# Kernel tuning notes

Measured on AMD Instinct MI355X. Metric: run time of the kernel, lower is better.

The kernel has to match this reference:

```python
import jax, jax.numpy as jnp
import numpy as np

DIM = 1024
NUM_HEADS = 16
HEAD_DIM = DIM // NUM_HEADS
B, L = 2, 2048


def setup_inputs() -> dict:
    key = jax.random.key(0)
    k_x, k_qkv, k_pw, k_pb = jax.random.split(key, 4)
    x = jax.random.normal(k_x, (B, L, DIM), dtype=jnp.float32)
    # nn.Linear(dim, 3*dim, bias=False): weight [3*dim, dim]; y = x @ W.T
    w_qkv = jax.random.normal(k_qkv, (3 * DIM, DIM), dtype=jnp.float32) * (DIM ** -0.5)
    # nn.Linear(dim, dim) with bias
    w_proj = jax.random.normal(k_pw, (DIM, DIM), dtype=jnp.float32) * (DIM ** -0.5)
    b_proj = jax.random.normal(k_pb, (DIM,), dtype=jnp.float32) * 0.01
    return {"x": x, "w_qkv": w_qkv, "w_proj": w_proj, "b_proj": b_proj}


def reference(x, w_qkv, w_proj, b_proj):
    Bx, Lx, C = x.shape
    qkv = x @ w_qkv.T  # [B, L, 3C]
    qkv = qkv.reshape(Bx, Lx, 3, NUM_HEADS, HEAD_DIM)
    q = jnp.transpose(qkv[:, :, 0], (0, 2, 1, 3))  # [B, H, L, D]
    k = jnp.transpose(qkv[:, :, 1], (0, 2, 1, 3))
    v = jnp.transpose(qkv[:, :, 2], (0, 2, 1, 3))
    attn = jnp.einsum('bhqd,bhkd->bhqk', q, k) * (HEAD_DIM ** -0.5)
    attn = jax.nn.softmax(attn, axis=-1)
    out = jnp.einsum('bhqk,bhkd->bhqd', attn, v)  # [B, H, L, D]
    out = jnp.transpose(out, (0, 2, 1, 3)).reshape(Bx, Lx, C)
    return out @ w_proj.T + b_proj
```

## Files before the change

### kernel.cpp

```cpp
#include <hip/hip_runtime.h>

#define DIM 1024
#define NH 16
#define HD 64
#define BB 2
#define LL 2048
#define BL (BB*LL)
#define NQKV (3*DIM)

typedef __bf16 bf16;
typedef __bf16 bf16x4 __attribute__((ext_vector_type(4)));
typedef __bf16 bf16x8 __attribute__((ext_vector_type(8)));
typedef float  f32x4  __attribute__((ext_vector_type(4)));

#define QSCALE 0.1803368801111204f

typedef __attribute__((address_space(3))) unsigned int lds_u32;
typedef __attribute__((address_space(1))) unsigned int glb_u32;

__device__ __forceinline__ void gld_lds16(const bf16* g, bf16* l) {
    __builtin_amdgcn_global_load_lds((const glb_u32*)g, (lds_u32*)l, 16, 0, 0);
}

#define C0 (BL*DIM/4)
#define C1 (NQKV*DIM/4)
#define C2 (DIM*DIM/4)
__global__ __launch_bounds__(256) void cvt_all(const float* __restrict__ x,
        const float* __restrict__ wq, const float* __restrict__ wp,
        bf16* __restrict__ xb, bf16* __restrict__ wqb, bf16* __restrict__ wpb) {
    int i = blockIdx.x * 256 + threadIdx.x;
    const float* in; bf16* out; int j;
    if (i < C0)            { in = x;  out = xb;  j = i; }
    else if (i < C0 + C1)  { in = wq; out = wqb; j = i - C0; }
    else                   { in = wp; out = wpb; j = i - C0 - C1; }
    float4 f = ((const float4*)in)[j];
    bf16x4 o = { (bf16)f.x, (bf16)f.y, (bf16)f.z, (bf16)f.w };
    ((bf16x4*)out)[j] = o;
}

__global__ __launch_bounds__(256, 3) void gemm_qkv(
        const bf16* __restrict__ A, const bf16* __restrict__ W,
        bf16* __restrict__ Qb, bf16* __restrict__ Kb, bf16* __restrict__ VTb) {
    __shared__ bf16 As[128][64];
    __shared__ bf16 Bs[128][64];
    const int tid = threadIdx.x;
    const int w = tid >> 6, lane = tid & 63, quad = lane >> 4, l16 = lane & 15;
    const int n0 = blockIdx.x * 128, m0 = blockIdx.y * 128;
    const int wm = (w & 1) * 64, wn = (w >> 1) * 64;
    f32x4 acc[4][4] = {};
    for (int k0 = 0; k0 < DIM; k0 += 64) {
        #pragma unroll
        for (int i = 0; i < 4; ++i) {
            int cb = w * 256 + i * 64;
            int gc = cb + lane;
            int r = gc >> 3;
            int cs = (gc & 7) ^ (r & 7);
            gld_lds16(A + (size_t)(m0 + r) * DIM + k0 + cs*8, &As[0][0] + cb * 8);
            gld_lds16(W + (size_t)(n0 + r) * DIM + k0 + cs*8, &Bs[0][0] + cb * 8);
        }
        __syncthreads();
        #pragma unroll
        for (int kc = 0; kc < 2; ++kc) {
            bf16x8 af[4], bfr[4];
            #pragma unroll
            for (int t = 0; t < 4; ++t) {
                int rw = wn + t*16 + l16;
                int cw = (kc*4 + quad) ^ (rw & 7);
                af[t] = *(const bf16x8*)(&Bs[0][0] + rw*64 + cw*8);
                int rx = wm + t*16 + l16;
                int cx = (kc*4 + quad) ^ (rx & 7);
                bfr[t] = *(const bf16x8*)(&As[0][0] + rx*64 + cx*8);
            }
            #pragma unroll
            for (int tm = 0; tm < 4; ++tm)
                #pragma unroll
                for (int tn = 0; tn < 4; ++tn)
                    acc[tm][tn] = __builtin_amdgcn_mfma_f32_16x16x32_bf16(
                                      af[tm], bfr[tn], acc[tm][tn], 0, 0, 0);
        }
        __syncthreads();
    }
    const int which = n0 >> 10;
    #pragma unroll
    for (int tm = 0; tm < 4; ++tm) {
        int nb = n0 + wn + tm*16 + quad*4;
        int rem = nb & 1023, h = rem >> 6, db = rem & 63;
        #pragma unroll
        for (int tn = 0; tn < 4; ++tn) {
            int m = m0 + wm + tn*16 + l16;
            int b = m >> 11, l = m & 2047, bh = (b << 4) | h;
            if (which == 0) {
                bf16x4 q4 = { (bf16)(acc[tm][tn][0] * QSCALE),
                              (bf16)(acc[tm][tn][1] * QSCALE),
                              (bf16)(acc[tm][tn][2] * QSCALE),
                              (bf16)(acc[tm][tn][3] * QSCALE) };
                *(bf16x4*)(Qb + ((size_t)bh << 17) + ((size_t)l << 6) + db) = q4;
            } else if (which == 1) {
                bf16x4 k4 = { (bf16)acc[tm][tn][0], (bf16)acc[tm][tn][1],
                              (bf16)acc[tm][tn][2], (bf16)acc[tm][tn][3] };
                *(bf16x4*)(Kb + ((size_t)bh << 17) + ((size_t)l << 6) + db) = k4;
            } else {
                #pragma unroll
                for (int r = 0; r < 4; ++r)
                    VTb[((size_t)bh << 17) + ((size_t)(db + r) << 11) + l] =
                        (bf16)acc[tm][tn][r];
            }
        }
    }
}

__global__ __launch_bounds__(256, 3) void gemm_proj(
        const bf16* __restrict__ A, const bf16* __restrict__ W,
        const float* __restrict__ bias, float* __restrict__ out) {
    __shared__ bf16 As[128][64];
    __shared__ bf16 Bs[64][64];
    const int tid = threadIdx.x;
    const int w = tid >> 6, lane = tid & 63, quad = lane >> 4, l16 = lane & 15;
    const int n0 = blockIdx.x * 64, m0 = blockIdx.y * 128;
    const int wm = (w & 1) * 64, wn = (w >> 1) * 32;
    f32x4 acc[2][4] = {};
    for (int k0 = 0; k0 < DIM; k0 += 64) {
        #pragma unroll
        for (int i = 0; i < 4; ++i) {
            int cb = w * 256 + i * 64;
            int gc = cb + lane;
            int r = gc >> 3;
            int cs = (gc & 7) ^ (r & 7);
            gld_lds16(A + (size_t)(m0 + r) * DIM + k0 + cs*8, &As[0][0] + cb * 8);
        }
        #pragma unroll
        for (int i = 0; i < 2; ++i) {
            int cb = w * 128 + i * 64;
            int gc = cb + lane;
            int r = gc >> 3;
            int cs = (gc & 7) ^ (r & 7);
            gld_lds16(W + (size_t)(n0 + r) * DIM + k0 + cs*8, &Bs[0][0] + cb * 8);
        }
        __syncthreads();
        #pragma unroll
        for (int kc = 0; kc < 2; ++kc) {
            bf16x8 af[2], bfr[4];
            #pragma unroll
            for (int t = 0; t < 2; ++t) {
                int rw = wn + t*16 + l16;
                int cw = (kc*4 + quad) ^ (rw & 7);
                af[t] = *(const bf16x8*)(&Bs[0][0] + rw*64 + cw*8);
            }
            #pragma unroll
            for (int t = 0; t < 4; ++t) {
                int rx = wm + t*16 + l16;
                int cx = (kc*4 + quad) ^ (rx & 7);
                bfr[t] = *(const bf16x8*)(&As[0][0] + rx*64 + cx*8);
            }
            #pragma unroll
            for (int tm = 0; tm < 2; ++tm)
                #pragma unroll
                for (int tn = 0; tn < 4; ++tn)
                    acc[tm][tn] = __builtin_amdgcn_mfma_f32_16x16x32_bf16(
                                      af[tm], bfr[tn], acc[tm][tn], 0, 0, 0);
        }
        __syncthreads();
    }
    #pragma unroll
    for (int tm = 0; tm < 2; ++tm) {
        int nb = n0 + wn + tm*16 + quad*4;
        float4 b4 = *(const float4*)&bias[nb];
        #pragma unroll
        for (int tn = 0; tn < 4; ++tn) {
            int m = m0 + wm + tn*16 + l16;
            float4 o4 = { acc[tm][tn][0] + b4.x, acc[tm][tn][1] + b4.y,
                          acc[tm][tn][2] + b4.z, acc[tm][tn][3] + b4.w };
            *(float4*)(out + (size_t)m * DIM + nb) = o4;
        }
    }
}

__global__ __launch_bounds__(256, 2) void attn(
        const bf16* __restrict__ Qb, const bf16* __restrict__ Kb,
        const bf16* __restrict__ VTb, bf16* __restrict__ AO) {
    __shared__ bf16 Ks[2][64][64];
    __shared__ bf16 VTs[2][64][64];
    __shared__ bf16 Ps[2][4][32][72];
    const int tid = threadIdx.x;
    const int w = tid >> 6, lane = tid & 63, quad = lane >> 4, l16 = lane & 15;
    const int qt = blockIdx.x, bh = blockIdx.y;
    const bf16* Qg = Qb + ((size_t)bh << 17) + (size_t)(qt * 128) * 64;
    const bf16* Kg = Kb + ((size_t)bh << 17);
    const bf16* Vg = VTb + ((size_t)bh << 17);

    bf16x8 aq[2][2];
    #pragma unroll
    for (int sub = 0; sub < 2; ++sub)
        #pragma unroll
        for (int kc = 0; kc < 2; ++kc)
            aq[sub][kc] = *(const bf16x8*)(Qg + (size_t)(w*32 + sub*16 + l16) * 64
                                           + kc*32 + quad*8);

    bf16x8 onesf = {};
    if (l16 == 0)
        #pragma unroll
        for (int j = 0; j < 8; ++j) onesf[j] = (bf16)1.0f;

    f32x4 oacc[2][4] = {};
    f32x4 lacc[2] = {};

    auto stageK = [&](int kt, int buf) {
        #pragma unroll
        for (int i = 0; i < 2; ++i) {
            int gc = w*128 + i*64 + lane;
            int r = gc >> 3;
            int cs = (gc & 7) ^ (r & 7) ^ ((r >> 3) & 7);
            gld_lds16(Kg + (size_t)(kt*64 + r) * 64 + cs*8,
                      &Ks[buf][0][0] + (w*128 + i*64) * 8);
        }
    };
    auto stageV = [&](int kt, int buf) {
        #pragma unroll
        for (int i = 0; i < 2; ++i) {
            int gc = w*128 + i*64 + lane;
            int r = gc >> 3;
            int cs = (gc & 7) ^ (r & 7) ^ ((r >> 3) & 7);
            gld_lds16(Vg + (size_t)r * 2048 + kt*64 + cs*8,
                      &VTs[buf][0][0] + (w*128 + i*64) * 8);
        }
    };
    auto pv = [&](int pbuf) {
        #pragma unroll
        for (int kc = 0; kc < 2; ++kc) {
            bf16x8 ap[2];
            #pragma unroll
            for (int sub = 0; sub < 2; ++sub)
                ap[sub] = *(const bf16x8*)&Ps[pbuf][w][sub*16 + l16][kc*32 + quad*8];
            #pragma unroll
            for (int nt = 0; nt < 4; ++nt) {
                int row = nt*16 + l16;
                int cp = (kc*4 + quad) ^ (row & 7) ^ ((row >> 3) & 7);
                bf16x8 bv = *(const bf16x8*)(&VTs[pbuf][0][0] + row*64 + cp*8);
                #pragma unroll
                for (int sub = 0; sub < 2; ++sub)
                    oacc[sub][nt] = __builtin_amdgcn_mfma_f32_16x16x32_bf16(
                                        ap[sub], bv, oacc[sub][nt], 0, 0, 0);
            }
            #pragma unroll
            for (int sub = 0; sub < 2; ++sub)
                lacc[sub] = __builtin_amdgcn_mfma_f32_16x16x32_bf16(
                                ap[sub], onesf, lacc[sub], 0, 0, 0);
        }
    };

    stageK(0, 0);
    for (int kt = 0; kt < 32; ++kt) {
        const int cur = kt & 1;
        __syncthreads();
        if (kt < 31) stageK(kt + 1, cur ^ 1);
        stageV(kt, cur);

        f32x4 s[2][4] = {};
        #pragma unroll
        for (int kc = 0; kc < 2; ++kc)
            #pragma unroll
            for (int nt = 0; nt < 4; ++nt) {
                int row = 4*l16 + nt;
                int cp = (kc*4 + quad) ^ (row & 7) ^ ((row >> 3) & 7);
                bf16x8 bk = *(const bf16x8*)(&Ks[cur][0][0] + row*64 + cp*8);
                #pragma unroll
                for (int sub = 0; sub < 2; ++sub)
                    s[sub][nt] = __builtin_amdgcn_mfma_f32_16x16x32_bf16(
                                     aq[sub][kc], bk, s[sub][nt], 0, 0, 0);
            }

        if (kt > 0) pv(cur ^ 1);

        #pragma unroll
        for (int sub = 0; sub < 2; ++sub)
            #pragma unroll
            for (int r = 0; r < 4; ++r) {
                bf16x4 p4 = { (bf16)exp2f(s[sub][0][r]), (bf16)exp2f(s[sub][1][r]),
                              (bf16)exp2f(s[sub][2][r]), (bf16)exp2f(s[sub][3][r]) };
                *(bf16x4*)&Ps[cur][w][sub*16 + quad*4 + r][4*l16] = p4;
            }
    }
    __syncthreads();
    pv(1);

    const int b = bh >> 4, h = bh & 15;
    #pragma unroll
    for (int sub = 0; sub < 2; ++sub)
        #pragma unroll
        for (int r = 0; r < 4; ++r) {
            float l = __shfl(lacc[sub][r], quad * 16, 64);
            float inv = 1.0f / l;
            int lq = qt*128 + w*32 + sub*16 + quad*4 + r;
            size_t rowbase = ((size_t)(b * 2048 + lq)) * DIM + h * 64;
            #pragma unroll
            for (int nt = 0; nt < 4; ++nt)
                AO[rowbase + nt*16 + l16] = (bf16)(oacc[sub][nt][r] * inv);
        }
}

extern "C" void kernel_launch(void* const* d_in, const int* in_sizes, int n_in,
                              void* d_out, int out_size, void* d_ws, size_t ws_size,
                              hipStream_t stream) {
    const float* x      = (const float*)d_in[0];
    const float* w_qkv  = (const float*)d_in[1];
    const float* w_proj = (const float*)d_in[2];
    const float* b_proj = (const float*)d_in[3];
    float* out = (float*)d_out;
    char* ws = (char*)d_ws;

    bf16* xb  = (bf16*)(ws);
    bf16* wqb = (bf16*)(ws + ( 8u << 20));
    bf16* wpb = (bf16*)(ws + (14u << 20));
    bf16* Qb  = (bf16*)(ws + (16u << 20));
    bf16* Kb  = (bf16*)(ws + (24u << 20));
    bf16* VTb = (bf16*)(ws + (32u << 20));
    bf16* AOb = (bf16*)(ws + (40u << 20));

    cvt_all<<<(C0 + C1 + C2) / 256, 256, 0, stream>>>(x, w_qkv, w_proj, xb, wqb, wpb);
    gemm_qkv<<<dim3(NQKV/128, BL/128), 256, 0, stream>>>(xb, wqb, Qb, Kb, VTb);
    attn<<<dim3(LL/128, BB*NH),        256, 0, stream>>>(Qb, Kb, VTb, AOb);
    gemm_proj<<<dim3(DIM/64, BL/128),  256, 0, stream>>>(AOb, wpb, b_proj, out);
}
```

Baseline: 197.4 us.

## Keep softmax probabilities in registers by computing transposed S tiles

Computes S^T via MFMA with K as the A operand and Q as B, so each lane's exp2 outputs already form the A-operand fragment for the P·V MFMA. This drops the Ps shared-memory buffer and its LDS write/read round trip. The K LDS swizzle is adjusted to keep the new access pattern bank-conflict free. The loop is unrolled by two with ping-pong register arrays, which costs extra VGPRs and may hurt occupancy under launch_bounds(256,2).

```diff
diff --git a/kernel.cpp b/kernel.cpp
--- a/kernel.cpp
+++ b/kernel.cpp
@@ -180,7 +180,6 @@
         const bf16* __restrict__ VTb, bf16* __restrict__ AO) {
     __shared__ bf16 Ks[2][64][64];
     __shared__ bf16 VTs[2][64][64];
-    __shared__ bf16 Ps[2][4][32][72];
     const int tid = threadIdx.x;
     const int w = tid >> 6, lane = tid & 63, quad = lane >> 4, l16 = lane & 15;
     const int qt = blockIdx.x, bh = blockIdx.y;
@@ -192,9 +191,9 @@
     #pragma unroll
     for (int sub = 0; sub < 2; ++sub)
         #pragma unroll
-        for (int kc = 0; kc < 2; ++kc)
-            aq[sub][kc] = *(const bf16x8*)(Qg + (size_t)(w*32 + sub*16 + l16) * 64
-                                           + kc*32 + quad*8);
+        for (int kd = 0; kd < 2; ++kd)
+            aq[sub][kd] = *(const bf16x8*)(Qg + (size_t)(w*32 + sub*16 + l16) * 64
+                                           + kd*32 + quad*8);
 
     bf16x8 onesf = {};
     if (l16 == 0)
@@ -203,15 +202,16 @@
 
     f32x4 oacc[2][4] = {};
     f32x4 lacc[2] = {};
+    bf16x8 apA[2][2], apB[2][2];
 
     auto stageK = [&](int kt, int buf) {
         #pragma unroll
         for (int i = 0; i < 2; ++i) {
             int gc = w*128 + i*64 + lane;
             int r = gc >> 3;
-            int cs = (gc & 7) ^ (r & 7) ^ ((r >> 3) & 7);
+            int cs = (gc & 7) ^ (r & 7) ^ ((r >> 3) & 7) ^ ((r & 1) << 2);
             gld_lds16(Kg + (size_t)(kt*64 + r) * 64 + cs*8,
-                      &Ks[buf][0][0] + (w*128 + i*64) * 8);
+                      &Ks[buf][0][0] + gc * 8);
         }
     };
     auto stageV = [&](int kt, int buf) {
@@ -221,67 +221,74 @@
             int r = gc >> 3;
             int cs = (gc & 7) ^ (r & 7) ^ ((r >> 3) & 7);
             gld_lds16(Vg + (size_t)r * 2048 + kt*64 + cs*8,
-                      &VTs[buf][0][0] + (w*128 + i*64) * 8);
+                      &VTs[buf][0][0] + gc * 8);
         }
     };
-    auto pv = [&](int pbuf) {
-        #pragma unroll
-        for (int kc = 0; kc < 2; ++kc) {
-            bf16x8 ap[2];
-            #pragma unroll
-            for (int sub = 0; sub < 2; ++sub)
-                ap[sub] = *(const bf16x8*)&Ps[pbuf][w][sub*16 + l16][kc*32 + quad*8];
+    auto pv = [&](int pbuf, bf16x8 (&ap)[2][2]) {
+        #pragma unroll
+        for (int kk = 0; kk < 2; ++kk) {
             #pragma unroll
             for (int nt = 0; nt < 4; ++nt) {
                 int row = nt*16 + l16;
-                int cp = (kc*4 + quad) ^ (row & 7) ^ ((row >> 3) & 7);
+                int cp = (kk*4 + quad) ^ (row & 7) ^ ((row >> 3) & 7);
                 bf16x8 bv = *(const bf16x8*)(&VTs[pbuf][0][0] + row*64 + cp*8);
                 #pragma unroll
                 for (int sub = 0; sub < 2; ++sub)
                     oacc[sub][nt] = __builtin_amdgcn_mfma_f32_16x16x32_bf16(
-                                        ap[sub], bv, oacc[sub][nt], 0, 0, 0);
+                                        ap[sub][kk], bv, oacc[sub][nt], 0, 0, 0);
             }
             #pragma unroll
             for (int sub = 0; sub < 2; ++sub)
                 lacc[sub] = __builtin_amdgcn_mfma_f32_16x16x32_bf16(
-                                ap[sub], onesf, lacc[sub], 0, 0, 0);
+                                ap[sub][kk], onesf, lacc[sub], 0, 0, 0);
         }
     };
 
-    stageK(0, 0);
-    for (int kt = 0; kt < 32; ++kt) {
-        const int cur = kt & 1;
+    auto body = [&](int kt, int cur, bf16x8 (&apw)[2][2], bf16x8 (&apr)[2][2]) {
         __syncthreads();
         if (kt < 31) stageK(kt + 1, cur ^ 1);
         stageV(kt, cur);
 
-        f32x4 s[2][4] = {};
-        #pragma unroll
-        for (int kc = 0; kc < 2; ++kc)
-            #pragma unroll
-            for (int nt = 0; nt < 4; ++nt) {
-                int row = 4*l16 + nt;
-                int cp = (kc*4 + quad) ^ (row & 7) ^ ((row >> 3) & 7);
-                bf16x8 bk = *(const bf16x8*)(&Ks[cur][0][0] + row*64 + cp*8);
-                #pragma unroll
-                for (int sub = 0; sub < 2; ++sub)
-                    s[sub][nt] = __builtin_amdgcn_mfma_f32_16x16x32_bf16(
-                                     aq[sub][kc], bk, s[sub][nt], 0, 0, 0);
-            }
-
-        if (kt > 0) pv(cur ^ 1);
+        f32x4 s[2][2][2] = {};
+        #pragma unroll
+        for (int kk = 0; kk < 2; ++kk)
+            #pragma unroll
+            for (int u = 0; u < 2; ++u)
+                #pragma unroll
+                for (int kd = 0; kd < 2; ++kd) {
+                    int rk = kk*32 + ((l16 >> 2) << 3) + u*4 + (l16 & 3);
+                    int cs = (kd*4 + quad) ^ (rk & 7) ^ ((rk >> 3) & 7)
+                             ^ ((rk & 1) << 2);
+                    bf16x8 ak = *(const bf16x8*)(&Ks[cur][0][0] + rk*64 + cs*8);
+                    #pragma unroll
+                    for (int sub = 0; sub < 2; ++sub)
+                        s[sub][kk][u] = __builtin_amdgcn_mfma_f32_16x16x32_bf16(
+                                            ak, aq[sub][kd], s[sub][kk][u], 0, 0, 0);
+                }
+
+        if (kt > 0) pv(cur ^ 1, apr);
 
         #pragma unroll
         for (int sub = 0; sub < 2; ++sub)
             #pragma unroll
-            for (int r = 0; r < 4; ++r) {
-                bf16x4 p4 = { (bf16)exp2f(s[sub][0][r]), (bf16)exp2f(s[sub][1][r]),
-                              (bf16)exp2f(s[sub][2][r]), (bf16)exp2f(s[sub][3][r]) };
-                *(bf16x4*)&Ps[cur][w][sub*16 + quad*4 + r][4*l16] = p4;
-            }
+            for (int kk = 0; kk < 2; ++kk) {
+                bf16x8 p;
+                #pragma unroll
+                for (int u = 0; u < 2; ++u)
+                    #pragma unroll
+                    for (int r = 0; r < 4; ++r)
+                        p[u*4 + r] = (bf16)exp2f(s[sub][kk][u][r]);
+                apw[sub][kk] = p;
+            }
+    };
+
+    stageK(0, 0);
+    for (int kt2 = 0; kt2 < 32; kt2 += 2) {
+        body(kt2,     0, apA, apB);
+        body(kt2 + 1, 1, apB, apA);
     }
     __syncthreads();
-    pv(1);
+    pv(1, apB);
 
     const int b = bh >> 4, h = bh & 15;
     #pragma unroll
```

Result: faster. 186.8 us (-5.4%).
